# Kernel tuning notes

Measured on AMD Instinct MI355X. Metric: run time of the kernel, lower is better.

Reference implementation:

```python
import jax, jax.numpy as jnp
import numpy as np

P, N, M, B = 5, 30000, 50000, 256
T, C, L, ED, H, EMB, TD, NL = 13, 16, 3, 4, 128, 64, 5, 3
SRC = jnp.repeat(jnp.arange(P), P)  # edge type i = src*P + dst
DST = jnp.tile(jnp.arange(P), P)


def _affine(x, W, b):
    # x: [P, n, i], W: [P, i, o], b: [P, o]
    return jnp.einsum('pni,pio->pno', x, W) + b[:, None, :]


def _lrelu(x, s=0.01):
    return jnp.where(x >= 0, x, s * x)


def _gat(h, W, a_s, a_d, We, a_e, b, edge_index, edge_attr):
    # h: [P, N, H]; per-edge-type GATConv (heads=1, no self loops) then hetero 'max' aggregation
    hs, hd = h[SRC], h[DST]                       # [25, N, H]
    xl = jnp.einsum('enh,ehf->enf', hs, W)        # transformed source features
    xr = jnp.einsum('enh,ehf->enf', hd, W)
    als = jnp.einsum('enf,ef->en', xl, a_s)
    ald = jnp.einsum('enf,ef->en', xr, a_d)

    def per_type(xl_e, als_e, ald_e, ea, We_e, ae_e, ei):
        src, dst = ei[0], ei[1]
        alpha = als_e[src] + ald_e[dst] + (ea @ We_e) @ ae_e
        alpha = jnp.where(alpha >= 0, alpha, 0.2 * alpha)  # GAT negative_slope=0.2
        amax = jax.ops.segment_max(alpha, dst, num_segments=N)
        ex = jnp.exp(alpha - amax[dst])
        den = jax.ops.segment_sum(ex, dst, num_segments=N)
        w = ex / (den[dst] + 1e-16)
        return jax.ops.segment_sum(w[:, None] * xl_e[src], dst, num_segments=N)

    out = jax.vmap(per_type)(xl, als, ald, edge_attr, We, a_e, edge_index)
    out = out + b[:, None, :]
    return out.reshape(P, P, N, H).max(axis=0)  # HeteroConv aggr='max' over source types


def setup_inputs():
    key = jax.random.key(0)
    ks = iter(jax.random.split(key, 64))
    def nrm(shape, s=1.0):
        return jax.random.normal(next(ks), shape, dtype=jnp.float32) * s
    w = 0.05
    inp = {
        'x': nrm((P, N, T)),
        'cond_x': nrm((P, N, C + L)),
        'edge_attr': nrm((P * P, M, ED)),
        'timesteps': jax.random.uniform(next(ks), (B,), dtype=jnp.float32),
        'te1_W': nrm((1, TD), w), 'te1_b': nrm((TD,), w),
        'te2_W': nrm((TD, TD), w), 'te2_b': nrm((TD,), w),
        'emb_W': nrm((P, T + L, EMB), w), 'emb_b': nrm((P, EMB), w),
        'cemb_W': nrm((P, C, EMB), w), 'cemb_b': nrm((P, EMB), w),
        'pa_W': nrm((P, 2 * EMB, 2 * EMB), w), 'pa_b': nrm((P, 2 * EMB), w),
        'pc_W': nrm((P, 2 * EMB, EMB), w), 'pc_b': nrm((P, EMB), w),
        'sl0_W': nrm((P, EMB + TD, H), w), 'sl0_b': nrm((P, H), w),
        'sl12_W': nrm((2, P, H + TD, H), w), 'sl12_b': nrm((2, P, H), w),
        'slout_W': nrm((P, H + TD, T), w), 'slout_b': nrm((P, T), w),
        'gat_W': nrm((NL, P * P, H, H), w), 'gat_as': nrm((NL, P * P, H), w),
        'gat_ad': nrm((NL, P * P, H), w), 'gat_We': nrm((NL, P * P, ED, H), w),
        'gat_ae': nrm((NL, P * P, H), w), 'gat_b': nrm((NL, P * P, H), w),
        'xc_W': nrm((NL, P, H, H // 2), w), 'xc_b': nrm((NL, P, H // 2), w),
        'cc_W': nrm((NL, P, H, H // 2), w), 'cc_b': nrm((NL, P, H // 2), w),
        'ca_W': nrm((NL, P, H, H), w), 'ca_b': nrm((NL, P, H), w),
        'batch_idx': jax.random.randint(next(ks), (P, N), 0, B),
        'edge_index': jax.random.randint(next(ks), (P * P, 2, M), 0, N),
    }
    return inp


def reference(x, cond_x, edge_attr, timesteps, te1_W, te1_b, te2_W, te2_b,
              emb_W, emb_b, cemb_W, cemb_b, pa_W, pa_b, pc_W, pc_b,
              sl0_W, sl0_b, sl12_W, sl12_b, slout_W, slout_b,
              gat_W, gat_as, gat_ad, gat_We, gat_ae, gat_b,
              xc_W, xc_b, cc_W, cc_b, ca_W, ca_b, batch_idx, edge_index):
    # time embedding: Linear(1,TD) -> SiLU -> Linear(TD,TD)
    temb = jax.nn.silu(timesteps[:, None] @ te1_W + te1_b) @ te2_W + te2_b  # [B, TD]
    cond, latent = cond_x[..., :C], cond_x[..., C:]
    h = _affine(jnp.concatenate([x, latent], -1), emb_W, emb_b)            # [P,N,EMB]
    ce = _affine(cond, cemb_W, cemb_b)
    h = jnp.concatenate([h, ce], -1)                                       # [P,N,2EMB]
    h = jax.nn.sigmoid(_affine(h, pa_W, pa_b)) * h                         # attention pooling
    h = _affine(h, pc_W, pc_b)                                             # [P,N,EMB]
    nt = temb[batch_idx]                                                   # [P,N,TD]
    h = jnp.concatenate([h, nt], -1)
    for l in range(NL):
        if l > 0:
            h = jnp.concatenate([h, nt], -1)
        Wl, bl = (sl0_W, sl0_b) if l == 0 else (sl12_W[l - 1], sl12_b[l - 1])
        h = _lrelu(_affine(h, Wl, bl))                                     # [P,N,H]
        comm = _lrelu(_gat(h, gat_W[l], gat_as[l], gat_ad[l], gat_We[l], gat_ae[l], gat_b[l], edge_index, edge_attr))
        h = jnp.concatenate([_affine(h, xc_W[l], xc_b[l]), _affine(comm, cc_W[l], cc_b[l])], -1)
        h = h + jax.nn.sigmoid(_affine(h, ca_W[l], ca_b[l])) * h
    h = jnp.concatenate([h, nt], -1)
    return _affine(h, slout_W, slout_b)                                    # [P,N,T]
```

## Files before the change

kernel.cpp:

```cpp
#include <hip/hip_runtime.h>
#include <cstdio>

using bf8 = __attribute__((ext_vector_type(8))) short;
using f4v = __attribute__((ext_vector_type(4))) float;
typedef unsigned short u16;
typedef unsigned int u32;

#define DEV __device__ __forceinline__

DEV float bf2f(u16 u){ return __uint_as_float(((u32)u) << 16); }
DEV u16 f2bf(float f){ u32 u = __float_as_uint(f); return (u16)((u + 0x7fffu + ((u >> 16) & 1u)) >> 16); }
DEV float sigm(float v){ return 1.f / (1.f + __expf(-v)); }

constexpr int P5 = 5, NN = 30000, MM = 50000, NE = 25, BB = 256;
constexpr int KC = 96;
constexpr int RS = KC * 2 + 16;
constexpr int RSA = 272;
constexpr int NSEG = 10, SEG = MM / NSEG;

__global__ void temb_k(const float* ts, const float* w1, const float* b1,
                       const float* w2, const float* b2, float* temb){
  int i = blockIdx.x * blockDim.x + threadIdx.x;
  if (i >= BB) return;
  float t = ts[i]; float z[5];
#pragma unroll
  for (int j = 0; j < 5; ++j){ float u = t * w1[j] + b1[j]; z[j] = u * sigm(u); }
#pragma unroll
  for (int j2 = 0; j2 < 5; ++j2){
    float s = b2[j2];
#pragma unroll
    for (int j = 0; j < 5; ++j) s += z[j] * w2[j * 5 + j2];
    temb[i * 5 + j2] = s;
  }
}

__global__ void wtransE_k(const float* __restrict__ W, u16* __restrict__ Wt,
                          int Kreal, int Kpad, int Nreal, int Nalloc, int total){
  int idx = blockIdx.x * blockDim.x + threadIdx.x;
  if (idx >= total) return;
  int k = idx % Kpad;
  int t2 = idx / Kpad;
  int f = t2 % Nalloc;
  int b = t2 / Nalloc;
  float v = (k < Kreal && f < Nreal) ? W[((size_t)b * Kreal + k) * Nreal + f] : 0.f;
  Wt[idx] = f2bf(v);
}

__global__ void embw_k(const float* emb_W, const float* emb_b, const float* cemb_W, const float* cemb_b,
                       u16* Wc, float* bc){
  int b = blockIdx.x, f = threadIdx.x;
  for (int k = 0; k < 32; ++k){
    float v = 0.f;
    if (f < 64){ if (k < 16) v = emb_W[((size_t)b * 16 + k) * 64 + f]; }
    else       { if (k >= 16) v = cemb_W[((size_t)b * 16 + (k - 16)) * 64 + (f - 64)]; }
    Wc[((size_t)b * 128 + f) * 32 + k] = f2bf(v);
  }
  bc[b * 128 + f] = (f < 64) ? emb_b[b * 64 + f] : cemb_b[b * 64 + (f - 64)];
}

__global__ void gwtT_k(const float* __restrict__ gW, u16* __restrict__ gWt){
  int idx = blockIdx.x * blockDim.x + threadIdx.x;
  if (idx >= 75 * 128 * 128) return;
  int h = idx & 127, f = (idx >> 7) & 127, le = idx >> 14;
  gWt[idx] = f2bf(gW[(size_t)le * 16384 + h * 128 + f]);
}

__global__ void gatred_k(const float* gW, const float* gas, const float* gad,
                         const float* gWe, const float* gae,
                         float* wswd, float* eaw){
  int le = blockIdx.x; int h = threadIdx.x;
  const float* W = gW + (size_t)le * 16384;
  const float* as_ = gas + le * 128;
  const float* ad_ = gad + le * 128;
  float wsv = 0.f, wdv = 0.f;
  for (int f = 0; f < 128; ++f){
    float w = W[h * 128 + f];
    wsv += w * as_[f]; wdv += w * ad_[f];
  }
  wswd[le * 256 + h] = wsv;
  wswd[le * 256 + 128 + h] = wdv;
  if (h < 4){
    const float* We = gWe + (size_t)le * 512;
    const float* ae = gae + le * 128;
    float s = 0.f;
    for (int f = 0; f < 128; ++f) s += We[h * 128 + f] * ae[f];
    eaw[le * 4 + h] = s;
  }
}

__global__ void abuild_k(const float* x, const float* cx, u16* A0){
  int idx = blockIdx.x * blockDim.x + threadIdx.x;
  if (idx >= P5 * NN) return;
  const float* xr = x + (size_t)idx * 13;
  const float* cr = cx + (size_t)idx * 19;
  u16* a0 = A0 + (size_t)idx * 32;
#pragma unroll
  for (int i = 0; i < 13; ++i) a0[i] = f2bf(xr[i]);
#pragma unroll
  for (int i = 0; i < 3; ++i) a0[13 + i] = f2bf(cr[16 + i]);
#pragma unroll
  for (int i = 0; i < 16; ++i) a0[16 + i] = f2bf(cr[i]);
}

__global__ void ntfill_k(u16* buf, int pitch, int co, const int* bidx, const float* temb){
  int idx = blockIdx.x * blockDim.x + threadIdx.x;
  if (idx >= P5 * NN) return;
  int b = bidx[idx];
  u16* r = buf + (size_t)idx * pitch;
#pragma unroll
  for (int j = 0; j < 5; ++j) r[co + j] = f2bf(temb[b * 5 + j]);
  for (int j = co + 5; j < pitch; ++j) r[j] = 0;
}

__global__ __launch_bounds__(1024) void csr_cnt_k(const int* __restrict__ EI, u16* __restrict__ hseg){
  extern __shared__ int cntl[];
  int b = blockIdx.x; int e = b / NSEG, s = b - e * NSEG;
  int tid = threadIdx.x;
  for (int i = tid; i < NN; i += 1024) cntl[i] = 0;
  __syncthreads();
  const int* dstp = EI + (size_t)e * 2 * MM + MM;
  int m0 = s * SEG;
  for (int m = m0 + tid; m < m0 + SEG; m += 1024) atomicAdd(&cntl[dstp[m]], 1);
  __syncthreads();
  u16* hp = hseg + ((size_t)e * NSEG + s) * NN;
  for (int i = tid; i < NN; i += 1024) hp[i] = (u16)cntl[i];
}

__global__ __launch_bounds__(1024) void csr_b1_k(const u16* __restrict__ hseg, int* __restrict__ ctot){
  __shared__ int red[16];
  int e = blockIdx.x / 30, c = blockIdx.x % 30;
  int tid = threadIdx.x, lane = tid & 63;
  int d = c * 1000 + tid;
  int tot = 0;
  if (tid < 1000 && d < NN){
    const u16* hb = hseg + (size_t)e * NSEG * NN + d;
    for (int s = 0; s < NSEG; ++s) tot += hb[(size_t)s * NN];
  }
  int v = tot;
#pragma unroll
  for (int o = 32; o > 0; o >>= 1) v += __shfl_down(v, o, 64);
  if (lane == 0) red[tid >> 6] = v;
  __syncthreads();
  if (tid == 0){
    int u = 0;
#pragma unroll
    for (int i = 0; i < 16; ++i) u += red[i];
    ctot[e * 30 + c] = u;
  }
}

__global__ void csr_b2_k(const int* __restrict__ ctot, int* __restrict__ cbase, int* __restrict__ off){
  int e = blockIdx.x, lane = threadIdx.x;
  int v = (lane < 30) ? ctot[e * 30 + lane] : 0;
  int s = v;
#pragma unroll
  for (int o = 1; o < 32; o <<= 1){ int t = __shfl_up(s, o, 64); if (lane >= o) s += t; }
  if (lane < 30) cbase[e * 30 + lane] = s - v;
  if (lane == 29) off[(size_t)e * (NN + 1) + NN] = s;
}

__global__ __launch_bounds__(1024) void csr_b3_k(const u16* __restrict__ hseg, const int* __restrict__ cbase,
                                                 int* __restrict__ off, u32* __restrict__ bseg){
  __shared__ int wsum[16];
  int e = blockIdx.x / 30, c = blockIdx.x % 30;
  int tid = threadIdx.x, lane = tid & 63, wv = tid >> 6;
  int d = c * 1000 + tid;
  bool ok = (tid < 1000 && d < NN);
  int h[NSEG]; int tot = 0;
  if (ok){
    const u16* hb = hseg + (size_t)e * NSEG * NN + d;
#pragma unroll
    for (int s = 0; s < NSEG; ++s){ h[s] = hb[(size_t)s * NN]; tot += h[s]; }
  } else {
#pragma unroll
    for (int s = 0; s < NSEG; ++s) h[s] = 0;
  }
  int v = tot, s1 = v;
#pragma unroll
  for (int o = 1; o < 64; o <<= 1){ int t = __shfl_up(s1, o, 64); if (lane >= o) s1 += t; }
  if (lane == 63) wsum[wv] = s1;
  __syncthreads();
  if (wv == 0 && lane < 16){
    int t = wsum[lane];
#pragma unroll
    for (int o = 1; o < 16; o <<= 1){ int u = __shfl_up(t, o, 64); if (lane >= o) t += u; }
    wsum[lane] = t;
  }
  __syncthreads();
  int excl = ((wv > 0) ? wsum[wv - 1] : 0) + (s1 - v) + cbase[e * 30 + c];
  if (ok){
    off[(size_t)e * (NN + 1) + d] = excl;
    u32 b = (u32)excl;
    u32* bb = bseg + (size_t)e * NSEG * NN + d;
#pragma unroll
    for (int s = 0; s < NSEG; ++s){ bb[(size_t)s * NN] = b; b += (u32)h[s]; }
  }
}

__global__ __launch_bounds__(1024) void csr_fill_k(const int* __restrict__ EI, const u32* __restrict__ bseg,
                                                   int2* __restrict__ sm){
  extern __shared__ int cntl[];
  int b = blockIdx.x; int e = b / NSEG, s = b - e * NSEG;
  int tid = threadIdx.x;
  const u32* bp = bseg + ((size_t)e * NSEG + s) * NN;
  for (int i = tid; i < NN; i += 1024) cntl[i] = (int)bp[i];
  __syncthreads();
  const int* srcp = EI + (size_t)e * 2 * MM;
  const int* dstp = srcp + MM;
  int m0 = s * SEG;
  for (int m = m0 + tid; m < m0 + SEG; m += 1024){
    int d = dstp[m];
    int pos = atomicAdd(&cntl[d], 1);
    int2 v; v.x = srcp[m]; v.y = m;
    sm[(size_t)e * MM + pos] = v;
  }
}

__global__ void eadot_k(const float* __restrict__ ea, const float* __restrict__ eaw,
                        const int2* __restrict__ sm, float* __restrict__ eadot){
  int idx = blockIdx.x * blockDim.x + threadIdx.x;
  if (idx >= 3 * NE * MM) return;
  int l = idx / (NE * MM);
  int rem = idx - l * NE * MM;
  int e = rem / MM, pos = rem - e * MM;
  int m = sm[(size_t)e * MM + pos].y;
  const float* a4 = ea + ((size_t)e * MM + m) * 4;
  const float* ew = eaw + (size_t)(l * NE + e) * 4;
  eadot[idx] = a4[0] * ew[0] + a4[1] * ew[1] + a4[2] * ew[2] + a4[3] * ew[3];
}

__global__ __launch_bounds__(256) void dots2_k(const u16* __restrict__ hS, const float* __restrict__ wswd_l,
                                               float* __restrict__ als, float* __restrict__ ald){
  __shared__ u32 hl[64][65];
  __shared__ float wsl[10][129];
  int p = blockIdx.y;
  int n0 = blockIdx.x * 64;
  int tid = threadIdx.x;
  for (int i = tid; i < 10 * 128; i += 256){
    int col = i >> 7, k = i & 127;
    int e = (col < 5) ? (p * 5 + col) : ((col - 5) * 5 + p);
    wsl[col][k] = wswd_l[e * 256 + ((col < 5) ? 0 : 128) + k];
  }
  for (int i = tid; i < 64 * 64; i += 256){
    int r = i >> 6, kp = i & 63;
    int n = n0 + r;
    hl[r][kp] = (n < NN) ? ((const u32*)hS)[((size_t)p * NN + n) * 64 + kp] : 0u;
  }
  __syncthreads();
  int col = tid & 15, rbase = tid >> 4;
  if (col < 10){
#pragma unroll
    for (int pass = 0; pass < 4; ++pass){
      int r = rbase + pass * 16;
      int n = n0 + r;
      if (n >= NN) continue;
      float s = 0.f;
#pragma unroll
      for (int kp = 0; kp < 64; ++kp){
        u32 pr = hl[r][kp];
        s += bf2f((u16)(pr & 0xffffu)) * wsl[col][2 * kp]
           + bf2f((u16)(pr >> 16)) * wsl[col][2 * kp + 1];
      }
      if (col < 5) als[(size_t)(p * 5 + col) * NN + n] = s;
      else         ald[(size_t)((col - 5) * 5 + p) * NN + n] = s;
    }
  }
}

__global__ __launch_bounds__(256) void aexp_k(const float* __restrict__ als, const float* __restrict__ ald,
                                              const float* __restrict__ eadot_l, const int2* __restrict__ sm,
                                              const int* __restrict__ off, uint2* __restrict__ prec){
  int idx = blockIdx.x * blockDim.x + threadIdx.x;
  if (idx >= NE * NN) return;
  int e = idx / NN;
  int ro = off[(size_t)e + idx], re = off[(size_t)e + idx + 1];
  if (ro >= re) return;
  float av = ald[idx];
  const int2* sc = sm + (size_t)e * MM;
  const float* ed = eadot_l + (size_t)e * MM;
  const float* ale = als + (size_t)e * NN;
  float mx = -3.0e38f;
  for (int j = ro; j < re; ++j){
    float a = ale[sc[j].x] + av + ed[j];
    a = (a >= 0.f) ? a : 0.2f * a;
    mx = fmaxf(mx, a);
  }
  for (int j = ro; j < re; ++j){
    int src = sc[j].x;
    float a = ale[src] + av + ed[j];
    a = (a >= 0.f) ? a : 0.2f * a;
    uint2 pr; pr.x = (u32)src; pr.y = __float_as_uint(__expf(a - mx));
    prec[(size_t)e * MM + j] = pr;
  }
}

__global__ __launch_bounds__(256) void agg3_k(const u16* __restrict__ hS, const uint2* __restrict__ prec,
                                              const int* __restrict__ off, u16* __restrict__ agghB,
                                              int pd0, int npd){
  int l = threadIdx.x & 63, w = threadIdx.x >> 6;
  int n0 = blockIdx.x * 8 + w;
  int n1 = n0 + 4;
  int y = blockIdx.y;
  int ps = y / npd, e = ps * 5 + pd0 + (y - ps * npd);
  const uint2* pe = prec + (size_t)e * MM;
  const int* offe = off + (size_t)e * (NN + 1);
  const u32* hb = (const u32*)hS + (size_t)ps * NN * 64 + l;
  int ro0 = 0, ln0 = 0, ro1 = 0, ln1 = 0;
  if (n0 < NN){ ro0 = offe[n0]; ln0 = offe[n0 + 1] - ro0; }
  if (n1 < NN){ ro1 = offe[n1]; ln1 = offe[n1 + 1] - ro1; }
  float den0 = 0.f, a00 = 0.f, a01 = 0.f;
  float den1 = 0.f, a10 = 0.f, a11 = 0.f;
  int mx = (ln0 > ln1) ? ln0 : ln1;
  for (int t = 0; t < mx; ++t){
    if (t < ln0){
      uint2 pr = pe[ro0 + t];
      float ex = __uint_as_float(pr.y);
      u32 hv = hb[(size_t)pr.x * 64];
      den0 += ex; a00 += ex * bf2f((u16)(hv & 0xffffu)); a01 += ex * bf2f((u16)(hv >> 16));
    }
    if (t < ln1){
      uint2 pr = pe[ro1 + t];
      float ex = __uint_as_float(pr.y);
      u32 hv = hb[(size_t)pr.x * 64];
      den1 += ex; a10 += ex * bf2f((u16)(hv & 0xffffu)); a11 += ex * bf2f((u16)(hv >> 16));
    }
  }
  if (n0 < NN){
    float inv = 1.f / (den0 + 1e-16f);
    ((u32*)agghB)[((size_t)y * NN + n0) * 64 + l] = (u32)f2bf(a00 * inv) | ((u32)f2bf(a01 * inv) << 16);
  }
  if (n1 < NN){
    float inv = 1.f / (den1 + 1e-16f);
    ((u32*)agghB)[((size_t)y * NN + n1) * 64 + l] = (u32)f2bf(a10 * inv) | ((u32)f2bf(a11 * inv) << 16);
  }
}

template<int NF, int MI, int NJ, int EPI, bool ALRELU>
__global__ __launch_bounds__(256) void tgemm_k(const u16* __restrict__ A, const u16* __restrict__ Wt,
                                               const float* __restrict__ bias, void* __restrict__ out,
                                               const u16* __restrict__ X,
                                               int Kpad, int opitch, int ocol, int xpitch){
  constexpr int Nalloc = NF * 16;
  constexpr int WR = 128 / (MI * 16);
  constexpr int WC = 4 / WR;
  static_assert(WR * WC == 4 && NJ * WC * 16 == Nalloc, "wave tiling");
  extern __shared__ __align__(16) char smem[];
  float* Cs = (float*)smem;
  const int tid = threadIdx.x;
  const int l = tid & 63, w = tid >> 6;
  const int bz = blockIdx.z;
  const int r0 = blockIdx.x * 128;
  const int wr = w / WC, wc = w % WC;
  const size_t Ab = (size_t)bz * NN;

  f4v acc[MI][NJ];
#pragma unroll
  for (int i = 0; i < MI; ++i)
#pragma unroll
    for (int j = 0; j < NJ; ++j) acc[i][j] = f4v{0.f, 0.f, 0.f, 0.f};

  for (int kb = 0; kb < Kpad; kb += KC){
    int kc = Kpad - kb; if (kc > KC) kc = KC;
    int nseg = kc >> 3;
    for (int s = tid; s < 128 * nseg; s += 256){
      int r = s / nseg, c = s - r * nseg;
      int grow = r0 + r; if (grow > NN - 1) grow = NN - 1;
      uint4 v = *(const uint4*)(A + (Ab + grow) * Kpad + kb + c * 8);
      if (ALRELU){
        u32 pr[4] = {v.x, v.y, v.z, v.w};
#pragma unroll
        for (int q = 0; q < 4; ++q){
          float lo = bf2f((u16)(pr[q] & 0xffffu)), hi = bf2f((u16)(pr[q] >> 16));
          lo = lo >= 0.f ? lo : 0.01f * lo; hi = hi >= 0.f ? hi : 0.01f * hi;
          pr[q] = (u32)f2bf(lo) | ((u32)f2bf(hi) << 16);
        }
        v.x = pr[0]; v.y = pr[1]; v.z = pr[2]; v.w = pr[3];
      }
      *(uint4*)(smem + r * RS + c * 16) = v;
    }
    for (int s = tid; s < Nalloc * nseg; s += 256){
      int r = s / nseg, c = s - r * nseg;
      uint4 v = *(const uint4*)(Wt + ((size_t)bz * Nalloc + r) * Kpad + kb + c * 8);
      *(uint4*)(smem + 128 * RS + r * RS + c * 16) = v;
    }
    __syncthreads();
    int KI = kc >> 5;
    for (int k0 = 0; k0 < KI; ++k0){
      bf8 af[MI], bfr[NJ];
#pragma unroll
      for (int i = 0; i < MI; ++i){
        int row = wr * (MI * 16) + i * 16 + (l & 15);
        af[i] = *(const bf8*)(smem + row * RS + k0 * 64 + (l >> 4) * 16);
      }
#pragma unroll
      for (int j = 0; j < NJ; ++j){
        int col = wc * (NJ * 16) + j * 16 + (l & 15);
        bfr[j] = *(const bf8*)(smem + 128 * RS + col * RS + k0 * 64 + (l >> 4) * 16);
      }
#pragma unroll
      for (int i = 0; i < MI; ++i)
#pragma unroll
        for (int j = 0; j < NJ; ++j)
          acc[i][j] = __builtin_amdgcn_mfma_f32_16x16x32_bf16(af[i], bfr[j], acc[i][j], 0, 0, 0);
    }
    __syncthreads();
  }

  if (EPI == 4){
    int col = l & 15;
    if (col < 13){
#pragma unroll
      for (int i = 0; i < MI; ++i){
        float bv = bias[bz * 13 + col];
#pragma unroll
        for (int r = 0; r < 4; ++r){
          int grow = r0 + wr * (MI * 16) + i * 16 + (l >> 4) * 4 + r;
          if (grow < NN)
            ((float*)out)[((size_t)bz * NN + grow) * 13 + col] = acc[i][0][r] + bv;
        }
      }
    }
    return;
  }

#pragma unroll
  for (int i = 0; i < MI; ++i)
#pragma unroll
    for (int j = 0; j < NJ; ++j){
      int tcol = wc * (NJ * 16) + j * 16 + (l & 15);
      float bv = bias[bz * Nalloc + tcol];
#pragma unroll
      for (int r = 0; r < 4; ++r){
        int trow = wr * (MI * 16) + i * 16 + (l >> 4) * 4 + r;
        float v = acc[i][j][r] + bv;
        if (EPI == 2) v = v >= 0.f ? v : 0.01f * v;
        Cs[trow * Nalloc + tcol] = v;
      }
    }
  __syncthreads();
  constexpr int nsc = Nalloc / 4;
  u16* o16 = (u16*)out;
  for (int s = tid; s < 128 * nsc; s += 256){
    int r = s / nsc, c = s - r * nsc;
    int grow = r0 + r; if (grow >= NN) continue;
    float4 cv = *(const float4*)(Cs + r * Nalloc + c * 4);
    float v0 = cv.x, v1 = cv.y, v2 = cv.z, v3 = cv.w;
    if (EPI == 1){
      uint2 xv = *(const uint2*)(X + ((size_t)bz * NN + grow) * xpitch + c * 4);
      float x0 = bf2f((u16)(xv.x & 0xffffu)), x1 = bf2f((u16)(xv.x >> 16));
      float x2 = bf2f((u16)(xv.y & 0xffffu)), x3 = bf2f((u16)(xv.y >> 16));
      v0 = x0 * sigm(v0); v1 = x1 * sigm(v1); v2 = x2 * sigm(v2); v3 = x3 * sigm(v3);
    }
    uint2 ov;
    ov.x = (u32)f2bf(v0) | ((u32)f2bf(v1) << 16);
    ov.y = (u32)f2bf(v2) | ((u32)f2bf(v3) << 16);
    *(uint2*)(o16 + ((size_t)bz * NN + grow) * opitch + ocol + c * 4) = ov;
  }
}

__global__ __launch_bounds__(256) void tgatmm_k(const u16* __restrict__ agghB, const u16* __restrict__ gWt_l,
                                                const float* __restrict__ gb_l, u16* __restrict__ comm,
                                                int pd){
  extern __shared__ __align__(16) char smem[];
  char* As = smem;
  char* Bs = smem + 64 * RSA;
  float* Cs = (float*)smem;
  const int tid = threadIdx.x, l = tid & 63, w = tid >> 6;
  const int r0 = blockIdx.x * 64;
  const int wr = w >> 1, wc = w & 1;
  f4v vmax[2][4];
#pragma unroll 1
  for (int ps = 0; ps < 5; ++ps){
    int e = ps * 5 + pd;
    const u16* aggs = agghB + (size_t)ps * NN * 128;
    const u16* wb = gWt_l + (size_t)e * 16384;
    for (int s = tid; s < 64 * 16; s += 256){
      int r = s >> 4, c = s & 15;
      int grow = r0 + r; if (grow > NN - 1) grow = NN - 1;
      *(uint4*)(As + r * RSA + c * 16) = *(const uint4*)(aggs + (size_t)grow * 128 + c * 8);
    }
    for (int s = tid; s < 128 * 16; s += 256){
      int r = s >> 4, c = s & 15;
      *(uint4*)(Bs + r * RSA + c * 16) = *(const uint4*)(wb + r * 128 + c * 8);
    }
    __syncthreads();
    f4v acc[2][4];
#pragma unroll
    for (int i = 0; i < 2; ++i)
#pragma unroll
      for (int j = 0; j < 4; ++j) acc[i][j] = f4v{0.f, 0.f, 0.f, 0.f};
#pragma unroll
    for (int k0 = 0; k0 < 4; ++k0){
      bf8 af[2], bfr[4];
#pragma unroll
      for (int i = 0; i < 2; ++i)
        af[i] = *(const bf8*)(As + (wr * 32 + i * 16 + (l & 15)) * RSA + k0 * 64 + (l >> 4) * 16);
#pragma unroll
      for (int j = 0; j < 4; ++j)
        bfr[j] = *(const bf8*)(Bs + (wc * 64 + j * 16 + (l & 15)) * RSA + k0 * 64 + (l >> 4) * 16);
#pragma unroll
      for (int i = 0; i < 2; ++i)
#pragma unroll
        for (int j = 0; j < 4; ++j)
          acc[i][j] = __builtin_amdgcn_mfma_f32_16x16x32_bf16(af[i], bfr[j], acc[i][j], 0, 0, 0);
    }
    const float* be = gb_l + e * 128;
#pragma unroll
    for (int i = 0; i < 2; ++i)
#pragma unroll
      for (int j = 0; j < 4; ++j){
        int tcol = wc * 64 + j * 16 + (l & 15);
        float bv = be[tcol];
#pragma unroll
        for (int r = 0; r < 4; ++r){
          float cvv = acc[i][j][r] + bv;
          vmax[i][j][r] = (ps == 0) ? cvv : fmaxf(vmax[i][j][r], cvv);
        }
      }
    __syncthreads();
  }
#pragma unroll
  for (int i = 0; i < 2; ++i)
#pragma unroll
    for (int j = 0; j < 4; ++j){
      int tcol = wc * 64 + j * 16 + (l & 15);
#pragma unroll
      for (int r = 0; r < 4; ++r){
        int trow = wr * 32 + i * 16 + (l >> 4) * 4 + r;
        Cs[trow * 128 + tcol] = vmax[i][j][r];
      }
    }
  __syncthreads();
  for (int s = tid; s < 64 * 32; s += 256){
    int r = s >> 5, c = s & 31;
    int grow = r0 + r; if (grow >= NN) continue;
    float4 cv = *(const float4*)(Cs + r * 128 + c * 4);
    uint2 ov;
    ov.x = (u32)f2bf(cv.x) | ((u32)f2bf(cv.y) << 16);
    ov.y = (u32)f2bf(cv.z) | ((u32)f2bf(cv.w) << 16);
    *(uint2*)(comm + ((size_t)pd * NN + grow) * 128 + c * 4) = ov;
  }
}

__global__ __launch_bounds__(256) void fca_k(const u16* __restrict__ hS, const u16* __restrict__ comm,
                                             const u16* __restrict__ wxc_l, const float* __restrict__ bxc_l,
                                             const u16* __restrict__ wcc_l, const float* __restrict__ bcc_l,
                                             const u16* __restrict__ wca_l, const float* __restrict__ bca_l,
                                             const int* __restrict__ bidx, const float* __restrict__ temb,
                                             u16* __restrict__ hL){
  extern __shared__ __align__(16) char smem[];
  char* As = smem;
  char* H2 = smem + 64 * RSA;
  const int tid = threadIdx.x, l = tid & 63, wv = tid >> 6;
  const int wr = wv >> 1, wc = wv & 1;
  const int bz = blockIdx.z;
  const int r0 = blockIdx.x * 64;
  const size_t pb = (size_t)bz * NN;

  for (int s = tid; s < 64 * 16; s += 256){
    int r = s >> 4, c = s & 15;
    int grow = r0 + r; if (grow > NN - 1) grow = NN - 1;
    *(uint4*)(As + r * RSA + c * 16) = *(const uint4*)(hS + (pb + grow) * 128 + c * 8);
    *(uint4*)(H2 + r * RSA + c * 16) = *(const uint4*)(wxc_l + (size_t)bz * 8192 + r * 128 + c * 8);
  }
  __syncthreads();
  f4v acc_a[2][2], acc_b[2][2];
#pragma unroll
  for (int i = 0; i < 2; ++i)
#pragma unroll
    for (int j = 0; j < 2; ++j) acc_a[i][j] = f4v{0.f, 0.f, 0.f, 0.f};
#pragma unroll
  for (int k0 = 0; k0 < 4; ++k0){
    bf8 af[2], bfr[2];
#pragma unroll
    for (int i = 0; i < 2; ++i)
      af[i] = *(const bf8*)(As + (wr * 32 + i * 16 + (l & 15)) * RSA + k0 * 64 + (l >> 4) * 16);
#pragma unroll
    for (int j = 0; j < 2; ++j)
      bfr[j] = *(const bf8*)(H2 + (wc * 32 + j * 16 + (l & 15)) * RSA + k0 * 64 + (l >> 4) * 16);
#pragma unroll
    for (int i = 0; i < 2; ++i)
#pragma unroll
      for (int j = 0; j < 2; ++j)
        acc_a[i][j] = __builtin_amdgcn_mfma_f32_16x16x32_bf16(af[i], bfr[j], acc_a[i][j], 0, 0, 0);
  }
  __syncthreads();
  for (int s = tid; s < 64 * 16; s += 256){
    int r = s >> 4, c = s & 15;
    int grow = r0 + r; if (grow > NN - 1) grow = NN - 1;
    uint4 v = *(const uint4*)(comm + (pb + grow) * 128 + c * 8);
    u32 pr[4] = {v.x, v.y, v.z, v.w};
#pragma unroll
    for (int q = 0; q < 4; ++q){
      float lo = bf2f((u16)(pr[q] & 0xffffu)), hi = bf2f((u16)(pr[q] >> 16));
      lo = lo >= 0.f ? lo : 0.01f * lo; hi = hi >= 0.f ? hi : 0.01f * hi;
      pr[q] = (u32)f2bf(lo) | ((u32)f2bf(hi) << 16);
    }
    v.x = pr[0]; v.y = pr[1]; v.z = pr[2]; v.w = pr[3];
    *(uint4*)(As + r * RSA + c * 16) = v;
    *(uint4*)(H2 + r * RSA + c * 16) = *(const uint4*)(wcc_l + (size_t)bz * 8192 + r * 128 + c * 8);
  }
  __syncthreads();
#pragma unroll
  for (int i = 0; i < 2; ++i)
#pragma unroll
    for (int j = 0; j < 2; ++j) acc_b[i][j] = f4v{0.f, 0.f, 0.f, 0.f};
#pragma unroll
  for (int k0 = 0; k0 < 4; ++k0){
    bf8 af[2], bfr[2];
#pragma unroll
    for (int i = 0; i < 2; ++i)
      af[i] = *(const bf8*)(As + (wr * 32 + i * 16 + (l & 15)) * RSA + k0 * 64 + (l >> 4) * 16);
#pragma unroll
    for (int j = 0; j < 2; ++j)
      bfr[j] = *(const bf8*)(H2 + (wc * 32 + j * 16 + (l & 15)) * RSA + k0 * 64 + (l >> 4) * 16);
#pragma unroll
    for (int i = 0; i < 2; ++i)
#pragma unroll
      for (int j = 0; j < 2; ++j)
        acc_b[i][j] = __builtin_amdgcn_mfma_f32_16x16x32_bf16(af[i], bfr[j], acc_b[i][j], 0, 0, 0);
  }
  __syncthreads();
#pragma unroll
  for (int i = 0; i < 2; ++i)
#pragma unroll
    for (int j = 0; j < 2; ++j){
      int colL = wc * 32 + j * 16 + (l & 15);
      float bL = bxc_l[bz * 64 + colL];
      float bR = bcc_l[bz * 64 + colL];
#pragma unroll
      for (int r = 0; r < 4; ++r){
        int row = wr * 32 + i * 16 + (l >> 4) * 4 + r;
        *(u16*)(H2 + row * RSA + colL * 2)        = f2bf(acc_a[i][j][r] + bL);
        *(u16*)(H2 + row * RSA + (colL + 64) * 2) = f2bf(acc_b[i][j][r] + bR);
      }
    }
  for (int s = tid; s < 64 * 16; s += 256){
    int r = s >> 4, c = s & 15;
    *(uint4*)(As + r * RSA + c * 16) = *(const uint4*)(wca_l + (size_t)bz * 16384 + r * 128 + c * 8);
  }
  __syncthreads();
  f4v acc_g0[2][2], acc_g1[2][2];
#pragma unroll
  for (int i = 0; i < 2; ++i)
#pragma unroll
    for (int j = 0; j < 2; ++j) acc_g0[i][j] = f4v{0.f, 0.f, 0.f, 0.f};
#pragma unroll
  for (int k0 = 0; k0 < 4; ++k0){
    bf8 af[2], bfr[2];
#pragma unroll
    for (int i = 0; i < 2; ++i)
      af[i] = *(const bf8*)(H2 + (wr * 32 + i * 16 + (l & 15)) * RSA + k0 * 64 + (l >> 4) * 16);
#pragma unroll
    for (int j = 0; j < 2; ++j)
      bfr[j] = *(const bf8*)(As + (wc * 32 + j * 16 + (l & 15)) * RSA + k0 * 64 + (l >> 4) * 16);
#pragma unroll
    for (int i = 0; i < 2; ++i)
#pragma unroll
      for (int j = 0; j < 2; ++j)
        acc_g0[i][j] = __builtin_amdgcn_mfma_f32_16x16x32_bf16(af[i], bfr[j], acc_g0[i][j], 0, 0, 0);
  }
  __syncthreads();
  for (int s = tid; s < 64 * 16; s += 256){
    int r = s >> 4, c = s & 15;
    *(uint4*)(As + r * RSA + c * 16) = *(const uint4*)(wca_l + (size_t)bz * 16384 + (64 + r) * 128 + c * 8);
  }
  __syncthreads();
#pragma unroll
  for (int i = 0; i < 2; ++i)
#pragma unroll
    for (int j = 0; j < 2; ++j) acc_g1[i][j] = f4v{0.f, 0.f, 0.f, 0.f};
#pragma unroll
  for (int k0 = 0; k0 < 4; ++k0){
    bf8 af[2], bfr[2];
#pragma unroll
    for (int i = 0; i < 2; ++i)
      af[i] = *(const bf8*)(H2 + (wr * 32 + i * 16 + (l & 15)) * RSA + k0 * 64 + (l >> 4) * 16);
#pragma unroll
    for (int j = 0; j < 2; ++j)
      bfr[j] = *(const bf8*)(As + (wc * 32 + j * 16 + (l & 15)) * RSA + k0 * 64 + (l >> 4) * 16);
#pragma unroll
    for (int i = 0; i < 2; ++i)
#pragma unroll
      for (int j = 0; j < 2; ++j)
        acc_g1[i][j] = __builtin_amdgcn_mfma_f32_16x16x32_bf16(af[i], bfr[j], acc_g1[i][j], 0, 0, 0);
  }
  float vout0[2][2][4], vout1[2][2][4];
#pragma unroll
  for (int i = 0; i < 2; ++i)
#pragma unroll
    for (int j = 0; j < 2; ++j){
      int col0 = wc * 32 + j * 16 + (l & 15);
      float bv0 = bca_l[bz * 128 + col0];
      float bv1 = bca_l[bz * 128 + col0 + 64];
#pragma unroll
      for (int r = 0; r < 4; ++r){
        int row = wr * 32 + i * 16 + (l >> 4) * 4 + r;
        float xg0 = bf2f(*(const u16*)(H2 + row * RSA + col0 * 2));
        float xg1 = bf2f(*(const u16*)(H2 + row * RSA + (col0 + 64) * 2));
        vout0[i][j][r] = xg0 * (1.f + sigm(acc_g0[i][j][r] + bv0));
        vout1[i][j][r] = xg1 * (1.f + sigm(acc_g1[i][j][r] + bv1));
      }
    }
  __syncthreads();
#pragma unroll
  for (int i = 0; i < 2; ++i)
#pragma unroll
    for (int j = 0; j < 2; ++j){
      int col0 = wc * 32 + j * 16 + (l & 15);
#pragma unroll
      for (int r = 0; r < 4; ++r){
        int row = wr * 32 + i * 16 + (l >> 4) * 4 + r;
        *(u16*)(As + row * RSA + col0 * 2)        = f2bf(vout0[i][j][r]);
        *(u16*)(As + row * RSA + (col0 + 64) * 2) = f2bf(vout1[i][j][r]);
      }
    }
  __syncthreads();
  for (int s = tid; s < 64 * 40; s += 256){
    int r = s / 40, c = s - r * 40;
    int grow = r0 + r; if (grow >= NN) continue;
    if (c < 32){
      uint2 v = *(const uint2*)(As + r * RSA + c * 8);
      *(uint2*)(hL + (pb + grow) * 160 + c * 4) = v;
    } else {
      int b = bidx[pb + grow];
      int col0 = c * 4;
      u16 t[4];
#pragma unroll
      for (int q = 0; q < 4; ++q){
        int j = col0 + q - 128;
        t[q] = (j < 5) ? f2bf(temb[b * 5 + j]) : (u16)0;
      }
      uint2 ov;
      ov.x = (u32)t[0] | ((u32)t[1] << 16);
      ov.y = (u32)t[2] | ((u32)t[3] << 16);
      *(uint2*)(hL + (pb + grow) * 160 + col0) = ov;
    }
  }
}

constexpr size_t ALN(size_t x){ return (x + 255) & ~(size_t)255; }
constexpr size_t SZ_A0   = ALN((size_t)P5 * NN * 32 * 2);
constexpr size_t SZ_H0   = ALN((size_t)P5 * NN * 96 * 2);
constexpr size_t SZ_H128 = ALN((size_t)P5 * NN * 128 * 2);
constexpr size_t SZ_HL   = ALN((size_t)P5 * NN * 160 * 2);
constexpr size_t O_A0 = 0;
constexpr size_t O_H0 = O_A0 + SZ_A0;
constexpr size_t O_AGG = 0;
constexpr size_t O_HCAT = O_H0 + SZ_H0;
constexpr size_t O_HG = O_HCAT + SZ_H128;
constexpr size_t O_HS = O_HG + SZ_H128;
constexpr size_t O_HL = O_HS + SZ_H128;
constexpr size_t O_HSEG = 0;
constexpr size_t O_BSEG = O_HSEG + ALN((size_t)NE * NSEG * NN * 2);
constexpr size_t O_CTOT = O_BSEG + ALN((size_t)NE * NSEG * NN * 4);
constexpr size_t O_CBASE= O_CTOT + ALN((size_t)NE * 30 * 4);
constexpr size_t O_TEMB = O_HL + SZ_HL;
constexpr size_t O_WSWD = O_TEMB + ALN(256 * 5 * 4);
constexpr size_t O_EAW  = O_WSWD + ALN(75 * 256 * 4);
constexpr size_t O_OFFS = O_EAW + ALN(75 * 4 * 4);
constexpr size_t O_ALS  = O_OFFS + ALN((size_t)NE * (NN + 1) * 4);
constexpr size_t O_ALD  = O_ALS + ALN((size_t)NE * NN * 4);
constexpr size_t O_SM   = O_ALD + ALN((size_t)NE * NN * 4);
constexpr size_t O_EADOT= O_SM + ALN((size_t)NE * MM * 8);
constexpr size_t O_GWT  = O_EADOT + ALN((size_t)3 * NE * MM * 4);
constexpr size_t O_WCMB = O_GWT + ALN((size_t)75 * 16384 * 2);
constexpr size_t O_BCMB = O_WCMB + ALN((size_t)5 * 128 * 32 * 2);
constexpr size_t O_WPA  = O_BCMB + ALN((size_t)5 * 128 * 4);
constexpr size_t O_WPC  = O_WPA + ALN((size_t)5 * 128 * 128 * 2);
constexpr size_t O_WSL0 = O_WPC + ALN((size_t)5 * 64 * 128 * 2);
constexpr size_t O_WSL12= O_WSL0 + ALN((size_t)5 * 128 * 96 * 2);
constexpr size_t O_WSLO = O_WSL12 + ALN((size_t)10 * 128 * 160 * 2);
constexpr size_t O_WXC  = O_WSLO + ALN((size_t)5 * 16 * 160 * 2);
constexpr size_t O_WCC  = O_WXC + ALN((size_t)15 * 64 * 128 * 2);
constexpr size_t O_WCA  = O_WCC + ALN((size_t)15 * 64 * 128 * 2);
constexpr size_t O_PREC = O_WCA + ALN((size_t)15 * 128 * 128 * 2);
constexpr size_t WS_NEED= O_PREC + ALN((size_t)NE * MM * 8);

extern "C" void kernel_launch(void* const* d_in, const int* in_sizes, int n_in,
                              void* d_out, int out_size, void* d_ws, size_t ws_size,
                              hipStream_t stream){
  if (ws_size < WS_NEED){
    fprintf(stderr, "kernel_launch: ws too small: need %zu have %zu\n", WS_NEED, ws_size);
    return;
  }
  const float* x        = (const float*)d_in[0];
  const float* cond_x   = (const float*)d_in[1];
  const float* edge_attr= (const float*)d_in[2];
  const float* timesteps= (const float*)d_in[3];
  const float* te1_W = (const float*)d_in[4];
  const float* te1_b = (const float*)d_in[5];
  const float* te2_W = (const float*)d_in[6];
  const float* te2_b = (const float*)d_in[7];
  const float* emb_W = (const float*)d_in[8];
  const float* emb_b = (const float*)d_in[9];
  const float* cemb_W= (const float*)d_in[10];
  const float* cemb_b= (const float*)d_in[11];
  const float* pa_W  = (const float*)d_in[12];
  const float* pa_b  = (const float*)d_in[13];
  const float* pc_W  = (const float*)d_in[14];
  const float* pc_b  = (const float*)d_in[15];
  const float* sl0_W = (const float*)d_in[16];
  const float* sl0_b = (const float*)d_in[17];
  const float* sl12_W= (const float*)d_in[18];
  const float* sl12_b= (const float*)d_in[19];
  const float* slout_W=(const float*)d_in[20];
  const float* slout_b=(const float*)d_in[21];
  const float* gat_W = (const float*)d_in[22];
  const float* gat_as= (const float*)d_in[23];
  const float* gat_ad= (const float*)d_in[24];
  const float* gat_We= (const float*)d_in[25];
  const float* gat_ae= (const float*)d_in[26];
  const float* gat_b = (const float*)d_in[27];
  const float* xc_W  = (const float*)d_in[28];
  const float* xc_b  = (const float*)d_in[29];
  const float* cc_W  = (const float*)d_in[30];
  const float* cc_b  = (const float*)d_in[31];
  const float* ca_W  = (const float*)d_in[32];
  const float* ca_b  = (const float*)d_in[33];
  const int* batch_idx = (const int*)d_in[34];
  const int* edge_index= (const int*)d_in[35];

  char* ws = (char*)d_ws;
  u16* A0    = (u16*)(ws + O_A0);
  u16* h0buf = (u16*)(ws + O_H0);
  u16* agghB = (u16*)(ws + O_AGG);
  u16* hcat  = (u16*)(ws + O_HCAT);
  u16* hg    = (u16*)(ws + O_HG);
  u16* comm  = (u16*)(ws + O_HG);
  u16* hS    = (u16*)(ws + O_HS);
  u16* hL    = (u16*)(ws + O_HL);
  u16* hseg  = (u16*)(ws + O_HSEG);
  u32* bseg  = (u32*)(ws + O_BSEG);
  int* ctot  = (int*)(ws + O_CTOT);
  int* cbase = (int*)(ws + O_CBASE);
  float* tembp = (float*)(ws + O_TEMB);
  float* wswdp = (float*)(ws + O_WSWD);
  float* eawp  = (float*)(ws + O_EAW);
  int* offs = (int*)(ws + O_OFFS);
  float* alsp = (float*)(ws + O_ALS);
  float* aldp = (float*)(ws + O_ALD);
  int2* smp  = (int2*)(ws + O_SM);
  float* eadotp = (float*)(ws + O_EADOT);
  u16* gwt   = (u16*)(ws + O_GWT);
  u16* wcmb  = (u16*)(ws + O_WCMB);
  float* bcmb= (float*)(ws + O_BCMB);
  u16* wpa   = (u16*)(ws + O_WPA);
  u16* wpc   = (u16*)(ws + O_WPC);
  u16* wsl0  = (u16*)(ws + O_WSL0);
  u16* wsl12 = (u16*)(ws + O_WSL12);
  u16* wslo  = (u16*)(ws + O_WSLO);
  u16* wxc   = (u16*)(ws + O_WXC);
  u16* wcc   = (u16*)(ws + O_WCC);
  u16* wca   = (u16*)(ws + O_WCA);
  uint2* precp = (uint2*)(ws + O_PREC);

  const dim3 B256(256);
  const dim3 TG(235, 1, 5);
  const int GPN = (P5 * NN + 255) / 256;
  const int GEN = (NE * NN + 255) / 256;
  constexpr int LDS_N128 = 65536;
  constexpr int LDS_N64  = 39936;
  constexpr int LDS_SLO  = 29952;
  constexpr int LDS_TGAT = 64 * RSA + 128 * RSA;
  constexpr int LDS_FCA  = 64 * RSA * 2;
  constexpr int LDS_CSR  = NN * 4;

  temb_k<<<1, B256, 0, stream>>>(timesteps, te1_W, te1_b, te2_W, te2_b, tembp);
  embw_k<<<5, 128, 0, stream>>>(emb_W, emb_b, cemb_W, cemb_b, wcmb, bcmb);
  {
    auto WT = [&](const float* W, u16* Wt, int Kr, int Kp, int Nr, int Na, int B){
      int total = B * Na * Kp;
      wtransE_k<<<(total + 255) / 256, B256, 0, stream>>>(W, Wt, Kr, Kp, Nr, Na, total);
    };
    WT(pa_W, wpa, 128, 128, 128, 128, 5);
    WT(pc_W, wpc, 128, 128, 64, 64, 5);
    WT(sl0_W, wsl0, 69, 96, 128, 128, 5);
    WT(sl12_W, wsl12, 133, 160, 128, 128, 10);
    WT(slout_W, wslo, 133, 160, 13, 16, 5);
    WT(xc_W, wxc, 128, 128, 64, 64, 15);
    WT(cc_W, wcc, 128, 128, 64, 64, 15);
    WT(ca_W, wca, 128, 128, 128, 128, 15);
  }
  gwtT_k<<<(75 * 128 * 128 + 255) / 256, B256, 0, stream>>>(gat_W, gwt);
  gatred_k<<<75, 128, 0, stream>>>(gat_W, gat_as, gat_ad, gat_We, gat_ae, wswdp, eawp);

  csr_cnt_k<<<NE * NSEG, 1024, LDS_CSR, stream>>>(edge_index, hseg);
  csr_b1_k<<<NE * 30, 1024, 0, stream>>>(hseg, ctot);
  csr_b2_k<<<NE, 64, 0, stream>>>(ctot, cbase, offs);
  csr_b3_k<<<NE * 30, 1024, 0, stream>>>(hseg, cbase, offs, bseg);
  csr_fill_k<<<NE * NSEG, 1024, LDS_CSR, stream>>>(edge_index, bseg, smp);
  eadot_k<<<(3 * NE * MM + 255) / 256, B256, 0, stream>>>(edge_attr, eawp, smp, eadotp);

  abuild_k<<<GPN, B256, 0, stream>>>(x, cond_x, A0);
  tgemm_k<8, 4, 4, 0, false><<<TG, B256, LDS_N128, stream>>>(A0, wcmb, bcmb, hcat, nullptr, 32, 128, 0, 0);
  tgemm_k<8, 4, 4, 1, false><<<TG, B256, LDS_N128, stream>>>(hcat, wpa, pa_b, hg, hcat, 128, 128, 0, 128);
  tgemm_k<4, 2, 4, 0, false><<<TG, B256, LDS_N64, stream>>>(hg, wpc, pc_b, h0buf, nullptr, 128, 96, 0, 0);
  ntfill_k<<<GPN, B256, 0, stream>>>(h0buf, 96, 64, batch_idx, tembp);

  for (int l = 0; l < 3; ++l){
    if (l == 0)
      tgemm_k<8, 4, 4, 2, false><<<TG, B256, LDS_N128, stream>>>(h0buf, wsl0, sl0_b, hS, nullptr, 96, 128, 0, 0);
    else
      tgemm_k<8, 4, 4, 2, false><<<TG, B256, LDS_N128, stream>>>(hL, wsl12 + (size_t)(l - 1) * 5 * 128 * 160,
                                                                 sl12_b + (size_t)(l - 1) * 5 * 128, hS, nullptr,
                                                                 160, 128, 0, 0);
    const float* wswd_l = wswdp + (size_t)l * 25 * 256;
    const u16* gwt_l = gwt + (size_t)l * 25 * 16384;
    const float* gb_l = gat_b + (size_t)l * 25 * 128;
    dots2_k<<<dim3(469, 5), B256, 0, stream>>>(hS, wswd_l, alsp, aldp);
    aexp_k<<<GEN, B256, 0, stream>>>(alsp, aldp, eadotp + (size_t)l * NE * MM, smp, offs, precp);
    for (int pd = 0; pd < 5; ++pd){
      agg3_k<<<dim3(3750, 5), B256, 0, stream>>>(hS, precp, offs, agghB, pd, 1);
      tgatmm_k<<<dim3(469), B256, LDS_TGAT, stream>>>(agghB, gwt_l, gb_l, comm, pd);
    }
    fca_k<<<dim3(469, 1, 5), B256, LDS_FCA, stream>>>(hS, comm,
        wxc + (size_t)l * 5 * 64 * 128, xc_b + (size_t)l * 5 * 64,
        wcc + (size_t)l * 5 * 64 * 128, cc_b + (size_t)l * 5 * 64,
        wca + (size_t)l * 5 * 128 * 128, ca_b + (size_t)l * 5 * 128,
        batch_idx, tembp, hL);
  }

  tgemm_k<1, 2, 1, 4, false><<<TG, B256, LDS_SLO, stream>>>(hL, wslo, slout_b, d_out, nullptr, 160, 13, 0, 0);
}
```

Baseline: 1.791 ms.

## Fuse GAT edge aggregation into per-destination-type matmul kernel via LDS

Replaces the agg3_k and tgatmm_k pair, previously launched per destination type, with a single fgat2_k kernel. Each block gathers softmax-weighted source features for its 64 rows directly into LDS, then runs the MFMA transform and max over source types. This removes the aggghB intermediate round trip through global memory and cuts ten launches per layer to one. The cost is fewer waves doing the irregular gather (8 rows per wave, serialized by the longest row) and gather latency that now sits in the same block as the GEMM, which may hurt latency hiding.

```diff
diff --git a/kernel.cpp b/kernel.cpp
--- a/kernel.cpp
+++ b/kernel.cpp
@@ -294,44 +294,119 @@
   }
 }
 
-__global__ __launch_bounds__(256) void agg3_k(const u16* __restrict__ hS, const uint2* __restrict__ prec,
-                                              const int* __restrict__ off, u16* __restrict__ agghB,
-                                              int pd0, int npd){
-  int l = threadIdx.x & 63, w = threadIdx.x >> 6;
-  int n0 = blockIdx.x * 8 + w;
-  int n1 = n0 + 4;
-  int y = blockIdx.y;
-  int ps = y / npd, e = ps * 5 + pd0 + (y - ps * npd);
-  const uint2* pe = prec + (size_t)e * MM;
-  const int* offe = off + (size_t)e * (NN + 1);
-  const u32* hb = (const u32*)hS + (size_t)ps * NN * 64 + l;
-  int ro0 = 0, ln0 = 0, ro1 = 0, ln1 = 0;
-  if (n0 < NN){ ro0 = offe[n0]; ln0 = offe[n0 + 1] - ro0; }
-  if (n1 < NN){ ro1 = offe[n1]; ln1 = offe[n1 + 1] - ro1; }
-  float den0 = 0.f, a00 = 0.f, a01 = 0.f;
-  float den1 = 0.f, a10 = 0.f, a11 = 0.f;
-  int mx = (ln0 > ln1) ? ln0 : ln1;
-  for (int t = 0; t < mx; ++t){
-    if (t < ln0){
-      uint2 pr = pe[ro0 + t];
-      float ex = __uint_as_float(pr.y);
-      u32 hv = hb[(size_t)pr.x * 64];
-      den0 += ex; a00 += ex * bf2f((u16)(hv & 0xffffu)); a01 += ex * bf2f((u16)(hv >> 16));
-    }
-    if (t < ln1){
-      uint2 pr = pe[ro1 + t];
-      float ex = __uint_as_float(pr.y);
-      u32 hv = hb[(size_t)pr.x * 64];
-      den1 += ex; a10 += ex * bf2f((u16)(hv & 0xffffu)); a11 += ex * bf2f((u16)(hv >> 16));
-    }
-  }
-  if (n0 < NN){
-    float inv = 1.f / (den0 + 1e-16f);
-    ((u32*)agghB)[((size_t)y * NN + n0) * 64 + l] = (u32)f2bf(a00 * inv) | ((u32)f2bf(a01 * inv) << 16);
-  }
-  if (n1 < NN){
-    float inv = 1.f / (den1 + 1e-16f);
-    ((u32*)agghB)[((size_t)y * NN + n1) * 64 + l] = (u32)f2bf(a10 * inv) | ((u32)f2bf(a11 * inv) << 16);
+__global__ __launch_bounds__(256) void fgat2_k(const u16* __restrict__ hS, const uint2* __restrict__ prec,
+                                               const int* __restrict__ off, const u16* __restrict__ gWt_l,
+                                               const float* __restrict__ gb_l, u16* __restrict__ comm){
+  extern __shared__ __align__(16) char smem[];
+  char* As = smem;
+  char* Bs = smem + 64 * RSA;
+  float* Cs = (float*)smem;
+  const int tid = threadIdx.x, l = tid & 63, w = tid >> 6;
+  const int pd = blockIdx.y;
+  const int r0 = blockIdx.x * 64;
+  const int wr = w >> 1, wc = w & 1;
+  f4v vmax[2][4];
+#pragma unroll 1
+  for (int ps = 0; ps < 5; ++ps){
+    int e = ps * 5 + pd;
+    const u16* wb = gWt_l + (size_t)e * 16384;
+    for (int s = tid; s < 128 * 16; s += 256){
+      int r = s >> 4, c = s & 15;
+      *(uint4*)(Bs + r * RSA + c * 16) = *(const uint4*)(wb + r * 128 + c * 8);
+    }
+    const uint2* pe = prec + (size_t)e * MM;
+    const int* offe = off + (size_t)e * (NN + 1);
+    const u32* hb = (const u32*)hS + (size_t)ps * NN * 64 + l;
+#pragma unroll 1
+    for (int g = 0; g < 2; ++g){
+      int rb = w * 16 + g * 8;
+      float den[8], s0[8], s1[8];
+      int ro[8], ln[8];
+      int mx = 0;
+#pragma unroll
+      for (int q = 0; q < 8; ++q){
+        int n = r0 + rb + q;
+        den[q] = 0.f; s0[q] = 0.f; s1[q] = 0.f;
+        if (n < NN){ ro[q] = offe[n]; ln[q] = offe[n + 1] - ro[q]; }
+        else { ro[q] = 0; ln[q] = 0; }
+        mx = (ln[q] > mx) ? ln[q] : mx;
+      }
+      for (int t = 0; t < mx; ++t){
+#pragma unroll
+        for (int q = 0; q < 8; ++q){
+          if (t < ln[q]){
+            uint2 pr = pe[ro[q] + t];
+            float ex = __uint_as_float(pr.y);
+            u32 hv = hb[(size_t)pr.x * 64];
+            den[q] += ex;
+            s0[q] += ex * bf2f((u16)(hv & 0xffffu));
+            s1[q] += ex * bf2f((u16)(hv >> 16));
+          }
+        }
+      }
+#pragma unroll
+      for (int q = 0; q < 8; ++q){
+        float inv = 1.f / (den[q] + 1e-16f);
+        u32 o = (u32)f2bf(s0[q] * inv) | ((u32)f2bf(s1[q] * inv) << 16);
+        *(u32*)(As + (rb + q) * RSA + l * 4) = o;
+      }
+    }
+    __syncthreads();
+    f4v acc[2][4];
+#pragma unroll
+    for (int i = 0; i < 2; ++i)
+#pragma unroll
+      for (int j = 0; j < 4; ++j) acc[i][j] = f4v{0.f, 0.f, 0.f, 0.f};
+#pragma unroll
+    for (int k0 = 0; k0 < 4; ++k0){
+      bf8 af[2], bfr[4];
+#pragma unroll
+      for (int i = 0; i < 2; ++i)
+        af[i] = *(const bf8*)(As + (wr * 32 + i * 16 + (l & 15)) * RSA + k0 * 64 + (l >> 4) * 16);
+#pragma unroll
+      for (int j = 0; j < 4; ++j)
+        bfr[j] = *(const bf8*)(Bs + (wc * 64 + j * 16 + (l & 15)) * RSA + k0 * 64 + (l >> 4) * 16);
+#pragma unroll
+      for (int i = 0; i < 2; ++i)
+#pragma unroll
+        for (int j = 0; j < 4; ++j)
+          acc[i][j] = __builtin_amdgcn_mfma_f32_16x16x32_bf16(af[i], bfr[j], acc[i][j], 0, 0, 0);
+    }
+    const float* be = gb_l + e * 128;
+#pragma unroll
+    for (int i = 0; i < 2; ++i)
+#pragma unroll
+      for (int j = 0; j < 4; ++j){
+        int tcol = wc * 64 + j * 16 + (l & 15);
+        float bv = be[tcol];
+#pragma unroll
+        for (int r = 0; r < 4; ++r){
+          float cvv = acc[i][j][r] + bv;
+          vmax[i][j][r] = (ps == 0) ? cvv : fmaxf(vmax[i][j][r], cvv);
+        }
+      }
+    __syncthreads();
+  }
+#pragma unroll
+  for (int i = 0; i < 2; ++i)
+#pragma unroll
+    for (int j = 0; j < 4; ++j){
+      int tcol = wc * 64 + j * 16 + (l & 15);
+#pragma unroll
+      for (int r = 0; r < 4; ++r){
+        int trow = wr * 32 + i * 16 + (l >> 4) * 4 + r;
+        Cs[trow * 128 + tcol] = vmax[i][j][r];
+      }
+    }
+  __syncthreads();
+  for (int s = tid; s < 64 * 32; s += 256){
+    int r = s >> 5, c = s & 31;
+    int grow = r0 + r; if (grow >= NN) continue;
+    float4 cv = *(const float4*)(Cs + r * 128 + c * 4);
+    uint2 ov;
+    ov.x = (u32)f2bf(cv.x) | ((u32)f2bf(cv.y) << 16);
+    ov.y = (u32)f2bf(cv.z) | ((u32)f2bf(cv.w) << 16);
+    *(uint2*)(comm + ((size_t)pd * NN + grow) * 128 + c * 4) = ov;
   }
 }
 
@@ -458,90 +533,6 @@
   }
 }
 
-__global__ __launch_bounds__(256) void tgatmm_k(const u16* __restrict__ agghB, const u16* __restrict__ gWt_l,
-                                                const float* __restrict__ gb_l, u16* __restrict__ comm,
-                                                int pd){
-  extern __shared__ __align__(16) char smem[];
-  char* As = smem;
-  char* Bs = smem + 64 * RSA;
-  float* Cs = (float*)smem;
-  const int tid = threadIdx.x, l = tid & 63, w = tid >> 6;
-  const int r0 = blockIdx.x * 64;
-  const int wr = w >> 1, wc = w & 1;
-  f4v vmax[2][4];
-#pragma unroll 1
-  for (int ps = 0; ps < 5; ++ps){
-    int e = ps * 5 + pd;
-    const u16* aggs = agghB + (size_t)ps * NN * 128;
-    const u16* wb = gWt_l + (size_t)e * 16384;
-    for (int s = tid; s < 64 * 16; s += 256){
-      int r = s >> 4, c = s & 15;
-      int grow = r0 + r; if (grow > NN - 1) grow = NN - 1;
-      *(uint4*)(As + r * RSA + c * 16) = *(const uint4*)(aggs + (size_t)grow * 128 + c * 8);
-    }
-    for (int s = tid; s < 128 * 16; s += 256){
-      int r = s >> 4, c = s & 15;
-      *(uint4*)(Bs + r * RSA + c * 16) = *(const uint4*)(wb + r * 128 + c * 8);
-    }
-    __syncthreads();
-    f4v acc[2][4];
-#pragma unroll
-    for (int i = 0; i < 2; ++i)
-#pragma unroll
-      for (int j = 0; j < 4; ++j) acc[i][j] = f4v{0.f, 0.f, 0.f, 0.f};
-#pragma unroll
-    for (int k0 = 0; k0 < 4; ++k0){
-      bf8 af[2], bfr[4];
-#pragma unroll
-      for (int i = 0; i < 2; ++i)
-        af[i] = *(const bf8*)(As + (wr * 32 + i * 16 + (l & 15)) * RSA + k0 * 64 + (l >> 4) * 16);
-#pragma unroll
-      for (int j = 0; j < 4; ++j)
-        bfr[j] = *(const bf8*)(Bs + (wc * 64 + j * 16 + (l & 15)) * RSA + k0 * 64 + (l >> 4) * 16);
-#pragma unroll
-      for (int i = 0; i < 2; ++i)
-#pragma unroll
-        for (int j = 0; j < 4; ++j)
-          acc[i][j] = __builtin_amdgcn_mfma_f32_16x16x32_bf16(af[i], bfr[j], acc[i][j], 0, 0, 0);
-    }
-    const float* be = gb_l + e * 128;
-#pragma unroll
-    for (int i = 0; i < 2; ++i)
-#pragma unroll
-      for (int j = 0; j < 4; ++j){
-        int tcol = wc * 64 + j * 16 + (l & 15);
-        float bv = be[tcol];
-#pragma unroll
-        for (int r = 0; r < 4; ++r){
-          float cvv = acc[i][j][r] + bv;
-          vmax[i][j][r] = (ps == 0) ? cvv : fmaxf(vmax[i][j][r], cvv);
-        }
-      }
-    __syncthreads();
-  }
-#pragma unroll
-  for (int i = 0; i < 2; ++i)
-#pragma unroll
-    for (int j = 0; j < 4; ++j){
-      int tcol = wc * 64 + j * 16 + (l & 15);
-#pragma unroll
-      for (int r = 0; r < 4; ++r){
-        int trow = wr * 32 + i * 16 + (l >> 4) * 4 + r;
-        Cs[trow * 128 + tcol] = vmax[i][j][r];
-      }
-    }
-  __syncthreads();
-  for (int s = tid; s < 64 * 32; s += 256){
-    int r = s >> 5, c = s & 31;
-    int grow = r0 + r; if (grow >= NN) continue;
-    float4 cv = *(const float4*)(Cs + r * 128 + c * 4);
-    uint2 ov;
-    ov.x = (u32)f2bf(cv.x) | ((u32)f2bf(cv.y) << 16);
-    ov.y = (u32)f2bf(cv.z) | ((u32)f2bf(cv.w) << 16);
-    *(uint2*)(comm + ((size_t)pd * NN + grow) * 128 + c * 4) = ov;
-  }
-}
-
 __global__ __launch_bounds__(256) void fca_k(const u16* __restrict__ hS, const u16* __restrict__ comm,
                                              const u16* __restrict__ wxc_l, const float* __restrict__ bxc_l,
                                              const u16* __restrict__ wcc_l, const float* __restrict__ bcc_l,
@@ -746,7 +737,6 @@
 constexpr size_t SZ_HL   = ALN((size_t)P5 * NN * 160 * 2);
 constexpr size_t O_A0 = 0;
 constexpr size_t O_H0 = O_A0 + SZ_A0;
-constexpr size_t O_AGG = 0;
 constexpr size_t O_HCAT = O_H0 + SZ_H0;
 constexpr size_t O_HG = O_HCAT + SZ_H128;
 constexpr size_t O_HS = O_HG + SZ_H128;
@@ -824,7 +814,6 @@
   char* ws = (char*)d_ws;
   u16* A0    = (u16*)(ws + O_A0);
   u16* h0buf = (u16*)(ws + O_H0);
-  u16* agghB = (u16*)(ws + O_AGG);
   u16* hcat  = (u16*)(ws + O_HCAT);
   u16* hg    = (u16*)(ws + O_HG);
   u16* comm  = (u16*)(ws + O_HG);
@@ -862,7 +851,7 @@
   constexpr int LDS_N128 = 65536;
   constexpr int LDS_N64  = 39936;
   constexpr int LDS_SLO  = 29952;
-  constexpr int LDS_TGAT = 64 * RSA + 128 * RSA;
+  constexpr int LDS_FGAT = 64 * RSA + 128 * RSA;
   constexpr int LDS_FCA  = 64 * RSA * 2;
   constexpr int LDS_CSR  = NN * 4;
 
@@ -910,10 +899,7 @@
     const float* gb_l = gat_b + (size_t)l * 25 * 128;
     dots2_k<<<dim3(469, 5), B256, 0, stream>>>(hS, wswd_l, alsp, aldp);
     aexp_k<<<GEN, B256, 0, stream>>>(alsp, aldp, eadotp + (size_t)l * NE * MM, smp, offs, precp);
-    for (int pd = 0; pd < 5; ++pd){
-      agg3_k<<<dim3(3750, 5), B256, 0, stream>>>(hS, precp, offs, agghB, pd, 1);
-      tgatmm_k<<<dim3(469), B256, LDS_TGAT, stream>>>(agghB, gwt_l, gb_l, comm, pd);
-    }
+    fgat2_k<<<dim3(469, 5), B256, LDS_FGAT, stream>>>(hS, precp, offs, gwt_l, gb_l, comm);
     fca_k<<<dim3(469, 1, 5), B256, LDS_FCA, stream>>>(hS, comm,
         wxc + (size_t)l * 5 * 64 * 128, xc_b + (size_t)l * 5 * 64,
         wcc + (size_t)l * 5 * 64 * 128, cc_b + (size_t)l * 5 * 64,
```

After: 2.115 ms. +18.0%, slower.
